# Performance work log

Measured on AMD Instinct MI355X. Metric: run time of the kernel, lower is better.

Reference implementation:

```python
import jax, jax.numpy as jnp
import numpy as np

N_NODES = 50000
N_EDGES = 800000
D_IN = 128
D_HID = 128   # initlial_net_sizes[-1]
D_GC = 128    # gc_out
D_OUT = 256   # feats_out


def setup_inputs() -> dict:
    key = jax.random.key(0)
    ks = jax.random.split(key, 8)
    feats = jax.random.normal(ks[0], (N_NODES, D_IN), dtype=jnp.float32)
    edges = jax.random.randint(ks[1], (2, N_EDGES), 0, N_NODES, dtype=jnp.int64)
    batch = jnp.sort(jax.random.randint(ks[2], (N_NODES,), 0, 64, dtype=jnp.int64))
    s = 0.05
    W1 = jax.random.normal(ks[3], (D_IN, D_HID), dtype=jnp.float32) * s
    b1 = jnp.zeros((D_HID,), dtype=jnp.float32)
    Wg = jax.random.normal(ks[4], (D_HID, D_GC), dtype=jnp.float32) * s
    bg = jnp.zeros((D_GC,), dtype=jnp.float32)
    W2 = jax.random.normal(ks[5], (D_HID + D_GC, D_OUT), dtype=jnp.float32) * s
    b2 = jnp.zeros((D_OUT,), dtype=jnp.float32)
    return {"feats": feats, "edges": edges, "batch": batch,
            "W1": W1, "b1": b1, "Wg": Wg, "bg": bg, "W2": W2, "b2": b2}


def _gcn_conv(x, edges, Wg, bg):
    # PyG GCNConv: linear -> add self-loops -> sym degree norm -> scatter-add -> bias
    n = x.shape[0]
    x = x @ Wg                                   # [N, D_GC]
    loop = jnp.arange(n, dtype=edges.dtype)
    src = jnp.concatenate([edges[0], loop])      # message source (x_j)
    dst = jnp.concatenate([edges[1], loop])      # aggregation target
    deg = jax.ops.segment_sum(jnp.ones_like(dst, dtype=x.dtype), dst, num_segments=n)
    dinv = jnp.where(deg > 0, jax.lax.rsqrt(deg), 0.0)
    norm = dinv[src] * dinv[dst]                 # [E+N]
    msg = x[src] * norm[:, None]                 # [E+N, D_GC]
    out = jax.ops.segment_sum(msg, dst, num_segments=n)
    return out + bg


def reference(feats, edges, batch, W1, b1, Wg, bg, W2, b2):
    nfeats = feats @ W1 + b1                     # fcnn (single Linear, no activation)
    gc_feats = _gcn_conv(nfeats, edges, Wg, bg)  # GCNConv
    combined = jnp.concatenate([nfeats, gc_feats], axis=1) @ W2 + b2
    return (combined, edges, batch)
```

## Files before the change

### kernel.cpp

```cpp
#include <hip/hip_runtime.h>
#include <hip/hip_bf16.h>
#include <stdint.h>


#define NND 50000
#define NE  800000

typedef unsigned int u32;
typedef unsigned short u16;
typedef unsigned long long u64;
typedef short bf16x8 __attribute__((ext_vector_type(8)));
typedef float f32x4  __attribute__((ext_vector_type(4)));

#define OFF_CSR  12800000
#define OFF_RNK  13200000
#define OFF_ROW  13600000
#define OFF_DEG  13700004
#define OFF_DINV 13750004
#define OFF_WPK2 13800004
#define OFF_WPK1 13832772
#define OFF_WPKG 13840964
#define OFF_BSUM 13849156

__device__ __forceinline__ float bf_lo(u32 u) { return __uint_as_float(u << 16); }
__device__ __forceinline__ float bf_hi(u32 u) { return __uint_as_float(u & 0xFFFF0000u); }
__device__ __forceinline__ unsigned short f2b(float f) {
    __hip_bfloat16 h = __float2bfloat16(f);
    return *(unsigned short*)&h;
}
__device__ __forceinline__ u32 pk2(float lo, float hi) {
    return ((u32)f2b(hi) << 16) | (u32)f2b(lo);
}

__device__ __forceinline__ int probe_isbf_par(const u32* p, int stride, int lane) {
    u32 v = p[lane * stride];
    u32 e = (v >> 7) & 0xFFu;
    u64 m = __ballot(e >= 90u && e <= 150u);
    return (__popcll(m) >= 40) ? 1 : 0;
}
__device__ __forceinline__ int probe_intfmt_par(const u32* p, int base, int stride, int lane) {
    int i = lane & 31;
    bool lo = lane < 32;
    u32 a = p[base + i * stride];
    u32 b = p[base + i * stride + 1];
    u32 e1 = (a >> 7) & 0xFFu;
    int small = __popcll(__ballot(lo && a < 50000u))
              + __popcll(__ballot(lo && b < 50000u));
    int oddz  = __popcll(__ballot(lo && b == 0u));
    int bfe   = __popcll(__ballot(lo && e1 >= 110u && e1 <= 145u));
    return (small >= 56) ? ((oddz >= 31) ? 1 : 0) : ((bfe >= 20) ? 3 : 2);
}

__device__ __forceinline__ int iread(const void* p, int fmt, int idx) {
    switch (fmt) {
        case 0:  return ((const int*)p)[idx];
        case 1:  return ((const int*)p)[2 * idx];
        case 2:  return (int)(((const float*)p)[idx] + 0.5f);
        default: return (int)(__bfloat162float(((const __hip_bfloat16*)p)[idx]) + 0.5f);
    }
}
__device__ __forceinline__ float fread_pass(const void* p, int fmt, int idx) {
    switch (fmt) {
        case 0:  return (float)((const int*)p)[idx];
        case 1:  return (float)((const int*)p)[2 * idx];
        case 2:  return ((const float*)p)[idx];
        default: return __bfloat162float(((const __hip_bfloat16*)p)[idx]);
    }
}
__device__ __forceinline__ float rdf(const void* p, int idx, int isbf) {
    return isbf ? __bfloat162float(((const __hip_bfloat16*)p)[idx])
                : ((const float*)p)[idx];
}
__device__ __forceinline__ float rdbias(const void* p, int idx) {
    return __bfloat162float(((const __hip_bfloat16*)p)[idx]);
}

__global__ __launch_bounds__(256) void k_degpack(
    const void* edges, const void* W1, const void* Wg, const void* W2,
    int* __restrict__ deg, u16* __restrict__ rank16,
    u16* __restrict__ Wpk1, u16* __restrict__ Wpkg, u16* __restrict__ Wpk2)
{
    int b = blockIdx.x, tid = threadIdx.x, lane = tid & 63;
    if (b < 3125) {
        int fmt = probe_intfmt_par((const u32*)edges, 0, 24992, lane);
        int e = b * 256 + tid;
        if (e < NE) {
            int s = iread(edges, fmt, e);
            int d = iread(edges, fmt, NE + e);
            if ((u32)s < (u32)NND && (u32)d < (u32)NND) {
                int r = atomicAdd(&deg[d], 1);
                rank16[e] = (u16)r;
            }
        }
    } else if (b < 3189) {
        int wbf = probe_isbf_par((const u32*)W1, 127, lane);
        int idx = (b - 3125) * 256 + tid;
        int j = idx & 7, l = (idx >> 3) & 63, nt = (idx >> 9) & 7, kk = (idx >> 12) & 3;
        int k = kk * 32 + ((l >> 4) & 3) * 8 + j;
        int n = nt * 16 + (l & 15);
        Wpk1[idx] = f2b(rdf(W1, k * 128 + n, wbf));
    } else if (b < 3253) {
        int wbf = probe_isbf_par((const u32*)Wg, 127, lane);
        int idx = (b - 3189) * 256 + tid;
        int j = idx & 7, l = (idx >> 3) & 63, nt = (idx >> 9) & 7, kk = (idx >> 12) & 3;
        int k = kk * 32 + ((l >> 4) & 3) * 8 + j;
        int n = nt * 16 + (l & 15);
        Wpkg[idx] = f2b(rdf(Wg, k * 128 + n, wbf));
    } else {
        int wbf = probe_isbf_par((const u32*)W2, 509, lane);
        int idx = (b - 3253) * 256 + tid;
        int j = idx & 7, l = (idx >> 3) & 63, nt = (idx >> 9) & 15, kk = idx >> 13;
        int k = kk * 32 + ((l >> 4) & 3) * 8 + j;
        int n = nt * 16 + (l & 15);
        Wpk2[idx] = f2b(rdf(W2, k * 256 + n, wbf));
    }
}

__global__ __launch_bounds__(256) void k_scannfxp(
    const int* __restrict__ deg, int* __restrict__ bsum,
    const void* feats, const u32* __restrict__ Wpk1, const u32* __restrict__ Wpkg,
    const void* b1, float* __restrict__ out, int M)
{
    __shared__ alignas(16) u32 smem[2048 + 2176];
    int b = blockIdx.x, tid = threadIdx.x;

    if (b < 196) {
        int* part = (int*)smem;
        int idx = b * 256 + tid;
        part[tid] = (idx < NND) ? deg[idx] : 0;
        __syncthreads();
        for (int off = 128; off >= 1; off >>= 1) {
            if (tid < off) part[tid] += part[tid + off];
            __syncthreads();
        }
        if (tid == 0) bsum[b] = part[0];
        return;
    }

    int nb = b - 196;
    int row0 = nb * 32;
    int lane = tid & 63, w = tid >> 6;
    u32* sApk = smem;
    uint4* sApk4 = (uint4*)smem;
    u16* nfl  = (u16*)(smem + 2048);

    int fbf = probe_isbf_par((const u32*)feats, 997, lane);

    if (fbf) {
        const u32* fw = (const u32*)feats;
        for (int i4 = tid; i4 < 512; i4 += 256) {
            int l = i4 & 63, kk = (i4 >> 6) & 3, mt = (i4 >> 8) & 1;
            int m = mt * 16 + (l & 15);
            int k0b = kk * 32 + ((l >> 4) & 3) * 8;
            int row = row0 + m;
            uint4 v = make_uint4(0u, 0u, 0u, 0u);
            if (row < M) v = *(const uint4*)&fw[(size_t)row * 64 + (k0b >> 1)];
            sApk4[i4] = v;
        }
    } else {
        const float* ff = (const float*)feats;
        for (int i4 = tid; i4 < 512; i4 += 256) {
            int l = i4 & 63, kk = (i4 >> 6) & 3, mt = (i4 >> 8) & 1;
            int m = mt * 16 + (l & 15);
            int k0b = kk * 32 + ((l >> 4) & 3) * 8;
            int row = row0 + m;
            uint4 v = make_uint4(0u, 0u, 0u, 0u);
            if (row < M) {
                float4 fa = *(const float4*)&ff[(size_t)row * 128 + k0b];
                float4 fb = *(const float4*)&ff[(size_t)row * 128 + k0b + 4];
                v = make_uint4(pk2(fa.x, fa.y), pk2(fa.z, fa.w),
                               pk2(fb.x, fb.y), pk2(fb.z, fb.w));
            }
            sApk4[i4] = v;
        }
    }
    __syncthreads();

    f32x4 acc[2][2];
#pragma unroll
    for (int mt = 0; mt < 2; ++mt)
#pragma unroll
        for (int t = 0; t < 2; ++t) acc[mt][t] = (f32x4){0.f, 0.f, 0.f, 0.f};

    for (int kk = 0; kk < 4; ++kk) {
        union { uint4 u; bf16x8 h; } ca0, ca1;
        ca0.u = *(const uint4*)&sApk[(kk * 64 + lane) * 4];
        ca1.u = *(const uint4*)&sApk[((4 + kk) * 64 + lane) * 4];
#pragma unroll
        for (int t = 0; t < 2; ++t) {
            int nt = w * 2 + t;
            union { uint4 u; bf16x8 h; } cb;
            cb.u = *(const uint4*)&Wpk1[((kk * 8 + nt) * 64 + lane) * 4];
            acc[0][t] = __builtin_amdgcn_mfma_f32_16x16x32_bf16(ca0.h, cb.h, acc[0][t], 0, 0, 0);
            acc[1][t] = __builtin_amdgcn_mfma_f32_16x16x32_bf16(ca1.h, cb.h, acc[1][t], 0, 0, 0);
        }
    }

    unsigned short* o16 = (unsigned short*)out;
    int q = lane >> 4, cn = lane & 15;
#pragma unroll
    for (int mt = 0; mt < 2; ++mt)
#pragma unroll
        for (int t = 0; t < 2; ++t) {
            int col = (w * 2 + t) * 16 + cn;
            float bb = rdbias(b1, col);
#pragma unroll
            for (int r = 0; r < 4; ++r) {
                int rowl = mt * 16 + q * 4 + r;
                int row = row0 + rowl;
                unsigned short v = f2b(acc[mt][t][r] + bb);
                nfl[rowl * 136 + col] = v;
                if (row < M) o16[(size_t)row * 512 + col] = v;
            }
        }
    __syncthreads();

    f32x4 acc2[2][2];
#pragma unroll
    for (int mt = 0; mt < 2; ++mt)
#pragma unroll
        for (int t = 0; t < 2; ++t) acc2[mt][t] = (f32x4){0.f, 0.f, 0.f, 0.f};

    for (int kk = 0; kk < 4; ++kk) {
        int kcol = kk * 32 + ((lane >> 4) & 3) * 8;
        union { uint4 u; bf16x8 h; } ca0, ca1;
        ca0.u = *(const uint4*)&nfl[(lane & 15) * 136 + kcol];
        ca1.u = *(const uint4*)&nfl[(16 + (lane & 15)) * 136 + kcol];
#pragma unroll
        for (int t = 0; t < 2; ++t) {
            int nt = w * 2 + t;
            union { uint4 u; bf16x8 h; } cb;
            cb.u = *(const uint4*)&Wpkg[((kk * 8 + nt) * 64 + lane) * 4];
            acc2[0][t] = __builtin_amdgcn_mfma_f32_16x16x32_bf16(ca0.h, cb.h, acc2[0][t], 0, 0, 0);
            acc2[1][t] = __builtin_amdgcn_mfma_f32_16x16x32_bf16(ca1.h, cb.h, acc2[1][t], 0, 0, 0);
        }
    }

#pragma unroll
    for (int mt = 0; mt < 2; ++mt)
#pragma unroll
        for (int t = 0; t < 2; ++t) {
            int col = (w * 2 + t) * 16 + cn;
#pragma unroll
            for (int r = 0; r < 4; ++r) {
                int row = row0 + mt * 16 + q * 4 + r;
                if (row < M)
                    o16[(size_t)row * 512 + 256 + col] = f2b(acc2[mt][t][r]);
            }
        }
}

__global__ __launch_bounds__(256) void k_scan23(
    const int* __restrict__ deg, const int* __restrict__ bsum,
    int* __restrict__ row_start, float* __restrict__ dinv)
{
    __shared__ int part[256];
    __shared__ int sboff;
    int t = threadIdx.x, b = blockIdx.x;

    int v = (t < 196) ? bsum[t] : 0;
    part[t] = v;
    __syncthreads();
    for (int off = 1; off < 256; off <<= 1) {
        int x = (t >= off) ? part[t - off] : 0;
        __syncthreads();
        part[t] += x;
        __syncthreads();
    }
    if (t == b) sboff = part[t] - v;
    if (b == 0 && t == 255) row_start[NND] = part[255];
    __syncthreads();
    int boffb = sboff;
    __syncthreads();

    int idx = b * 256 + t;
    int dv = (idx < NND) ? deg[idx] : 0;
    part[t] = dv;
    __syncthreads();
    for (int off = 1; off < 256; off <<= 1) {
        int x = (t >= off) ? part[t - off] : 0;
        __syncthreads();
        part[t] += x;
        __syncthreads();
    }
    if (idx < NND) {
        int rs = boffb + part[t] - dv;
        row_start[idx] = rs;
        dinv[idx] = rsqrtf((float)(dv + 1));
    }
}

__global__ __launch_bounds__(256) void k_place(const void* edges,
                                               const int* __restrict__ row_start,
                                               const u16* __restrict__ rank16,
                                               u16* __restrict__ csr16)
{
    int fmt = probe_intfmt_par((const u32*)edges, 0, 24992, threadIdx.x & 63);
    int e = blockIdx.x * 256 + threadIdx.x;
    if (e < NE) {
        int s = iread(edges, fmt, e);
        int d = iread(edges, fmt, NE + e);
        if ((u32)s < (u32)NND && (u32)d < (u32)NND) {
            int pos = row_start[d] + (int)rank16[e];
            csr16[pos] = (u16)s;
        }
    }
}

__global__ __launch_bounds__(256) void k_gather(
    const u16* __restrict__ csr16, const int* __restrict__ row_start,
    const float* __restrict__ dinv, const void* bg, u32* __restrict__ uw)
{
    int gt = blockIdx.x * 256 + threadIdx.x;
    int node = gt >> 6, l = gt & 63;
    if (node >= NND) return;
    int beg = row_start[node], end = row_start[node + 1];

    u32 us = uw[(size_t)node * 256 + 128 + l];
    float di = dinv[node];
    float bg0 = rdbias(bg, 2 * l);
    float bg1 = rdbias(bg, 2 * l + 1);

    float a0 = 0.f, a1 = 0.f;
    float c0 = 0.f, c1 = 0.f;
    int e0 = end - 1;
    for (int i = beg; i < end; i += 8) {
        int j1 = i + 1, j2 = i + 2, j3 = i + 3;
        int j4 = i + 4, j5 = i + 5, j6 = i + 6, j7 = i + 7;
        int s0 = csr16[i];
        int s1 = csr16[j1 < e0 ? j1 : e0];
        int s2 = csr16[j2 < e0 ? j2 : e0];
        int s3 = csr16[j3 < e0 ? j3 : e0];
        int s4 = csr16[j4 < e0 ? j4 : e0];
        int s5 = csr16[j5 < e0 ? j5 : e0];
        int s6 = csr16[j6 < e0 ? j6 : e0];
        int s7 = csr16[j7 < e0 ? j7 : e0];
        u32 u0 = uw[(size_t)s0 * 256 + 128 + l];
        u32 u1 = uw[(size_t)s1 * 256 + 128 + l];
        u32 u2 = uw[(size_t)s2 * 256 + 128 + l];
        u32 u3 = uw[(size_t)s3 * 256 + 128 + l];
        u32 u4 = uw[(size_t)s4 * 256 + 128 + l];
        u32 u5 = uw[(size_t)s5 * 256 + 128 + l];
        u32 u6 = uw[(size_t)s6 * 256 + 128 + l];
        u32 u7 = uw[(size_t)s7 * 256 + 128 + l];
        float w0 = dinv[s0];
        float w1 = (j1 <= e0) ? dinv[s1] : 0.f;
        float w2 = (j2 <= e0) ? dinv[s2] : 0.f;
        float w3 = (j3 <= e0) ? dinv[s3] : 0.f;
        float w4 = (j4 <= e0) ? dinv[s4] : 0.f;
        float w5 = (j5 <= e0) ? dinv[s5] : 0.f;
        float w6 = (j6 <= e0) ? dinv[s6] : 0.f;
        float w7 = (j7 <= e0) ? dinv[s7] : 0.f;
        a0 = fmaf(w0, bf_lo(u0), a0); a1 = fmaf(w0, bf_hi(u0), a1);
        c0 = fmaf(w1, bf_lo(u1), c0); c1 = fmaf(w1, bf_hi(u1), c1);
        a0 = fmaf(w2, bf_lo(u2), a0); a1 = fmaf(w2, bf_hi(u2), a1);
        c0 = fmaf(w3, bf_lo(u3), c0); c1 = fmaf(w3, bf_hi(u3), c1);
        a0 = fmaf(w4, bf_lo(u4), a0); a1 = fmaf(w4, bf_hi(u4), a1);
        c0 = fmaf(w5, bf_lo(u5), c0); c1 = fmaf(w5, bf_hi(u5), c1);
        a0 = fmaf(w6, bf_lo(u6), a0); a1 = fmaf(w6, bf_hi(u6), a1);
        c0 = fmaf(w7, bf_lo(u7), c0); c1 = fmaf(w7, bf_hi(u7), c1);
    }
    a0 += c0; a1 += c1;
    float g0 = di * (a0 + di * bf_lo(us)) + bg0;
    float g1 = di * (a1 + di * bf_hi(us)) + bg1;
    uw[(size_t)node * 256 + 192 + l] = ((u32)f2b(g1) << 16) | (u32)f2b(g0);
}

__global__ __launch_bounds__(256) void k_final(
    const u32* __restrict__ Wpk, const void* b2, float* __restrict__ out, int M)
{
    __shared__ alignas(16) u32 sApk[4096];
    uint4* sApk4 = (uint4*)sApk;
    int tid = threadIdx.x;
    int row0 = blockIdx.x * 32;
    const u32* uw = (const u32*)out;

    for (int i4 = tid; i4 < 1024; i4 += 256) {
        int l = i4 & 63, kk = (i4 >> 6) & 7, mt = (i4 >> 9) & 1;
        int m = mt * 16 + (l & 15);
        int k0b = kk * 32 + ((l >> 4) & 3) * 8;
        int row = row0 + m;
        uint4 v = make_uint4(0u, 0u, 0u, 0u);
        if (row < M) {
            size_t base = (kk < 4)
                ? (size_t)row * 256 + (k0b >> 1)
                : (size_t)row * 256 + 192 + ((k0b - 128) >> 1);
            v = *(const uint4*)&uw[base];
        }
        sApk4[i4] = v;
    }
    __syncthreads();

    int w = tid >> 6, lane = tid & 63;
    f32x4 acc[2][4];
#pragma unroll
    for (int mt = 0; mt < 2; ++mt)
#pragma unroll
        for (int t = 0; t < 4; ++t) acc[mt][t] = (f32x4){0.f, 0.f, 0.f, 0.f};

    for (int kk = 0; kk < 8; ++kk) {
        union { uint4 u; bf16x8 h; } ca0, ca1;
        ca0.u = *(const uint4*)&sApk[(kk * 64 + lane) * 4];
        ca1.u = *(const uint4*)&sApk[((8 + kk) * 64 + lane) * 4];
#pragma unroll
        for (int t = 0; t < 4; ++t) {
            int nt = w * 4 + t;
            union { uint4 u; bf16x8 h; } cb;
            cb.u = *(const uint4*)&Wpk[((size_t)(kk * 16 + nt) * 64 + lane) * 4];
            acc[0][t] = __builtin_amdgcn_mfma_f32_16x16x32_bf16(ca0.h, cb.h, acc[0][t], 0, 0, 0);
            acc[1][t] = __builtin_amdgcn_mfma_f32_16x16x32_bf16(ca1.h, cb.h, acc[1][t], 0, 0, 0);
        }
    }

    int q = lane >> 4, cn = lane & 15;
#pragma unroll
    for (int mt = 0; mt < 2; ++mt)
#pragma unroll
        for (int t = 0; t < 4; ++t) {
            int col = w * 64 + t * 16 + cn;
            float bb = rdbias(b2, col);
#pragma unroll
            for (int r = 0; r < 4; ++r) {
                int row = row0 + mt * 16 + q * 4 + r;
                if (row < M) {
                    float v = acc[mt][t][r] + bb;
                    if (!(fabsf(v) < 900.f)) v = (v == v) ? copysignf(900.f, v) : 0.f;
                    out[(size_t)row * 256 + col] = v;
                }
            }
        }
}

__global__ __launch_bounds__(256) void k_tail(
    const void* edges, const void* batch, float* __restrict__ out)
{
    int lane = threadIdx.x & 63;
    int f0 = probe_intfmt_par((const u32*)edges, 0, 24992, lane);
    int f1 = probe_intfmt_par((const u32*)batch, 20000, 156, lane);
    int T = blockIdx.x * 256 + threadIdx.x;
    if (T < NE) {
        size_t o = (size_t)NND * 256 + 2 * (size_t)T;
        if (f0 == 1) {
            int4 v = ((const int4*)edges)[T];
            *(float2*)&out[o] = make_float2((float)v.x, (float)v.z);
        } else {
            out[o]     = fread_pass(edges, f0, 2 * T);
            out[o + 1] = fread_pass(edges, f0, 2 * T + 1);
        }
    } else if (T < NE + NND / 2) {
        int U = T - NE;
        size_t o = (size_t)NND * 256 + 2 * (size_t)NE + 2 * (size_t)U;
        if (f1 == 1) {
            int4 v = ((const int4*)batch)[U];
            *(float2*)&out[o] = make_float2((float)v.x, (float)v.z);
        } else {
            out[o]     = fread_pass(batch, f1, 2 * U);
            out[o + 1] = fread_pass(batch, f1, 2 * U + 1);
        }
    }
}

extern "C" void kernel_launch(void* const* d_in, const int* in_sizes, int n_in,
                              void* d_out, int out_size, void* d_ws, size_t ws_size,
                              hipStream_t stream)
{
    int i_feats = -1, i_edges = -1, i_batch = -1, i_W1 = -1, i_Wg = -1,
        i_W2 = -1, i_b1 = -1, i_bg = -1, i_b2 = -1;
    for (int i = 0; i < n_in; ++i) {
        int s = in_sizes[i];
        if      (s == 6400000) i_feats = i;
        else if (s == 1600000) i_edges = i;
        else if (s == 50000)   i_batch = i;
        else if (s == 65536)   i_W2 = i;
        else if (s == 256)     i_b2 = i;
        else if (s == 16384)   { if (i_W1 < 0) i_W1 = i; else i_Wg = i; }
        else if (s == 128)     { if (i_b1 < 0) i_b1 = i; else i_bg = i; }
    }
    if (i_feats < 0 || i_edges < 0 || i_batch < 0 || i_W1 < 0 || i_Wg < 0 ||
        i_W2 < 0 || i_b1 < 0 || i_bg < 0 || i_b2 < 0) {
        i_feats = 0; i_edges = 1; i_batch = 2; i_W1 = 3; i_b1 = 4;
        i_Wg = 5; i_bg = 6; i_W2 = 7; i_b2 = 8;
    }
    const void* feats = d_in[i_feats];
    const void* edges = d_in[i_edges];
    const void* batch = d_in[i_batch];
    const void* W1 = d_in[i_W1];
    const void* b1 = d_in[i_b1];
    const void* Wg = d_in[i_Wg];
    const void* bg = d_in[i_bg];
    const void* W2 = d_in[i_W2];
    const void* b2 = d_in[i_b2];

    float* out = (float*)d_out;
    u16*   csr16     = (u16*)  (out + OFF_CSR);
    u16*   rank16    = (u16*)  (out + OFF_RNK);
    int*   row_start = (int*)  (out + OFF_ROW);
    int*   deg       = (int*)  (out + OFF_DEG);
    float* dinv      = (float*)(out + OFF_DINV);
    u16*   Wpk2 = (u16*)(out + OFF_WPK2);
    u16*   Wpk1 = (u16*)(out + OFF_WPK1);
    u16*   Wpkg = (u16*)(out + OFF_WPKG);
    int*   bsum = (int*)(out + OFF_BSUM);

    hipMemsetAsync(deg, 0, 200000, stream);
    k_degpack <<<3509,  256, 0, stream>>>(edges, W1, Wg, W2, deg, rank16,
                                          Wpk1, Wpkg, Wpk2);
    k_scannfxp<<<1759,  256, 0, stream>>>(deg, bsum, feats, (const u32*)Wpk1,
                                          (const u32*)Wpkg, b1, out, NND);
    k_scan23  <<<196,   256, 0, stream>>>(deg, bsum, row_start, dinv);
    k_place   <<<3125,  256, 0, stream>>>(edges, row_start, rank16, csr16);
    k_gather  <<<12500, 256, 0, stream>>>(csr16, row_start, dinv, bg, (u32*)out);
    k_final   <<<1563,  256, 0, stream>>>((const u32*)Wpk2, b2, out, NND);
    k_tail    <<<3224,  256, 0, stream>>>(edges, batch, out);
}
```

Measured before the change: 221.7 us.

## Restructure prologue kernels: fold memset into weight pack, merge degree count with node GEMM

Weight packing and zeroing the degree array now run together in a small kernel ahead of everything else, replacing the separate memset. Degree counting now shares a launch with the feature/GCN-linear GEMM, because that GEMM only needs the packed weights and not the degrees. The block-sum pass is removed: each scan block recomputes its prefix offset by summing all earlier degree chunks directly. This removes one launch and one memset, at the cost of scan blocks doing redundant reads whose amount grows with block index.

```diff
diff --git a/kernel.cpp b/kernel.cpp
--- a/kernel.cpp
+++ b/kernel.cpp
@@ -20,7 +20,6 @@
 #define OFF_WPK2 13800004
 #define OFF_WPK1 13832772
 #define OFF_WPKG 13840964
-#define OFF_BSUM 13849156
 
 __device__ __forceinline__ float bf_lo(u32 u) { return __uint_as_float(u << 16); }
 __device__ __forceinline__ float bf_hi(u32 u) { return __uint_as_float(u & 0xFFFF0000u); }
@@ -75,12 +74,48 @@
     return __bfloat162float(((const __hip_bfloat16*)p)[idx]);
 }
 
-__global__ __launch_bounds__(256) void k_degpack(
-    const void* edges, const void* W1, const void* Wg, const void* W2,
+__global__ __launch_bounds__(256) void k_pack(
+    const void* W1, const void* Wg, const void* W2,
+    u16* __restrict__ Wpk1, u16* __restrict__ Wpkg, u16* __restrict__ Wpk2,
+    int* __restrict__ deg)
+{
+    int b = blockIdx.x, tid = threadIdx.x, lane = tid & 63;
+    if (b < 64) {
+        int wbf = probe_isbf_par((const u32*)W1, 127, lane);
+        int idx = b * 256 + tid;
+        int j = idx & 7, l = (idx >> 3) & 63, nt = (idx >> 9) & 7, kk = (idx >> 12) & 3;
+        int k = kk * 32 + ((l >> 4) & 3) * 8 + j;
+        int n = nt * 16 + (l & 15);
+        Wpk1[idx] = f2b(rdf(W1, k * 128 + n, wbf));
+    } else if (b < 128) {
+        int wbf = probe_isbf_par((const u32*)Wg, 127, lane);
+        int idx = (b - 64) * 256 + tid;
+        int j = idx & 7, l = (idx >> 3) & 63, nt = (idx >> 9) & 7, kk = (idx >> 12) & 3;
+        int k = kk * 32 + ((l >> 4) & 3) * 8 + j;
+        int n = nt * 16 + (l & 15);
+        Wpkg[idx] = f2b(rdf(Wg, k * 128 + n, wbf));
+    } else if (b < 384) {
+        int wbf = probe_isbf_par((const u32*)W2, 509, lane);
+        int idx = (b - 128) * 256 + tid;
+        int j = idx & 7, l = (idx >> 3) & 63, nt = (idx >> 9) & 15, kk = idx >> 13;
+        int k = kk * 32 + ((l >> 4) & 3) * 8 + j;
+        int n = nt * 16 + (l & 15);
+        Wpk2[idx] = f2b(rdf(W2, k * 256 + n, wbf));
+    } else {
+        int idx = (b - 384) * 256 + tid;
+        if (idx < 12500) ((int4*)deg)[idx] = make_int4(0, 0, 0, 0);
+    }
+}
+
+__global__ __launch_bounds__(256) void k_degnfxp(
+    const void* edges, const void* feats,
+    const u32* __restrict__ Wpk1, const u32* __restrict__ Wpkg, const void* b1,
     int* __restrict__ deg, u16* __restrict__ rank16,
-    u16* __restrict__ Wpk1, u16* __restrict__ Wpkg, u16* __restrict__ Wpk2)
-{
+    float* __restrict__ out, int M)
+{
+    __shared__ alignas(16) u32 smem[2048 + 2176];
     int b = blockIdx.x, tid = threadIdx.x, lane = tid & 63;
+
     if (b < 3125) {
         int fmt = probe_intfmt_par((const u32*)edges, 0, 24992, lane);
         int e = b * 256 + tid;
@@ -92,54 +127,12 @@
                 rank16[e] = (u16)r;
             }
         }
-    } else if (b < 3189) {
-        int wbf = probe_isbf_par((const u32*)W1, 127, lane);
-        int idx = (b - 3125) * 256 + tid;
-        int j = idx & 7, l = (idx >> 3) & 63, nt = (idx >> 9) & 7, kk = (idx >> 12) & 3;
-        int k = kk * 32 + ((l >> 4) & 3) * 8 + j;
-        int n = nt * 16 + (l & 15);
-        Wpk1[idx] = f2b(rdf(W1, k * 128 + n, wbf));
-    } else if (b < 3253) {
-        int wbf = probe_isbf_par((const u32*)Wg, 127, lane);
-        int idx = (b - 3189) * 256 + tid;
-        int j = idx & 7, l = (idx >> 3) & 63, nt = (idx >> 9) & 7, kk = (idx >> 12) & 3;
-        int k = kk * 32 + ((l >> 4) & 3) * 8 + j;
-        int n = nt * 16 + (l & 15);
-        Wpkg[idx] = f2b(rdf(Wg, k * 128 + n, wbf));
-    } else {
-        int wbf = probe_isbf_par((const u32*)W2, 509, lane);
-        int idx = (b - 3253) * 256 + tid;
-        int j = idx & 7, l = (idx >> 3) & 63, nt = (idx >> 9) & 15, kk = idx >> 13;
-        int k = kk * 32 + ((l >> 4) & 3) * 8 + j;
-        int n = nt * 16 + (l & 15);
-        Wpk2[idx] = f2b(rdf(W2, k * 256 + n, wbf));
-    }
-}
-
-__global__ __launch_bounds__(256) void k_scannfxp(
-    const int* __restrict__ deg, int* __restrict__ bsum,
-    const void* feats, const u32* __restrict__ Wpk1, const u32* __restrict__ Wpkg,
-    const void* b1, float* __restrict__ out, int M)
-{
-    __shared__ alignas(16) u32 smem[2048 + 2176];
-    int b = blockIdx.x, tid = threadIdx.x;
-
-    if (b < 196) {
-        int* part = (int*)smem;
-        int idx = b * 256 + tid;
-        part[tid] = (idx < NND) ? deg[idx] : 0;
-        __syncthreads();
-        for (int off = 128; off >= 1; off >>= 1) {
-            if (tid < off) part[tid] += part[tid + off];
-            __syncthreads();
-        }
-        if (tid == 0) bsum[b] = part[0];
         return;
     }
 
-    int nb = b - 196;
+    int nb = b - 3125;
     int row0 = nb * 32;
-    int lane = tid & 63, w = tid >> 6;
+    int w = tid >> 6;
     u32* sApk = smem;
     uint4* sApk4 = (uint4*)smem;
     u16* nfl  = (u16*)(smem + 2048);
@@ -250,16 +243,30 @@
         }
 }
 
-__global__ __launch_bounds__(256) void k_scan23(
-    const int* __restrict__ deg, const int* __restrict__ bsum,
+__global__ __launch_bounds__(256) void k_scan(
+    const int* __restrict__ deg,
     int* __restrict__ row_start, float* __restrict__ dinv)
 {
     __shared__ int part[256];
-    __shared__ int sboff;
+    __shared__ int stot;
     int t = threadIdx.x, b = blockIdx.x;
 
-    int v = (t < 196) ? bsum[t] : 0;
-    part[t] = v;
+    int acc = 0;
+    for (int c = 0; c < b; ++c) acc += deg[c * 256 + t];
+    part[t] = acc;
+    __syncthreads();
+    for (int off = 128; off >= 1; off >>= 1) {
+        if (t < off) part[t] += part[t + off];
+        __syncthreads();
+    }
+    if (t == 0) stot = part[0];
+    __syncthreads();
+    int S_b = stot;
+    __syncthreads();
+
+    int idx = b * 256 + t;
+    int dv = (idx < NND) ? deg[idx] : 0;
+    part[t] = dv;
     __syncthreads();
     for (int off = 1; off < 256; off <<= 1) {
         int x = (t >= off) ? part[t - off] : 0;
@@ -267,27 +274,12 @@
         part[t] += x;
         __syncthreads();
     }
-    if (t == b) sboff = part[t] - v;
-    if (b == 0 && t == 255) row_start[NND] = part[255];
-    __syncthreads();
-    int boffb = sboff;
-    __syncthreads();
-
-    int idx = b * 256 + t;
-    int dv = (idx < NND) ? deg[idx] : 0;
-    part[t] = dv;
-    __syncthreads();
-    for (int off = 1; off < 256; off <<= 1) {
-        int x = (t >= off) ? part[t - off] : 0;
-        __syncthreads();
-        part[t] += x;
-        __syncthreads();
-    }
     if (idx < NND) {
-        int rs = boffb + part[t] - dv;
+        int rs = S_b + part[t] - dv;
         row_start[idx] = rs;
         dinv[idx] = rsqrtf((float)(dv + 1));
     }
+    if (b == 195 && t == 255) row_start[NND] = S_b + part[255];
 }
 
 __global__ __launch_bounds__(256) void k_place(const void* edges,
@@ -500,14 +492,12 @@
     u16*   Wpk2 = (u16*)(out + OFF_WPK2);
     u16*   Wpk1 = (u16*)(out + OFF_WPK1);
     u16*   Wpkg = (u16*)(out + OFF_WPKG);
-    int*   bsum = (int*)(out + OFF_BSUM);
-
-    hipMemsetAsync(deg, 0, 200000, stream);
-    k_degpack <<<3509,  256, 0, stream>>>(edges, W1, Wg, W2, deg, rank16,
-                                          Wpk1, Wpkg, Wpk2);
-    k_scannfxp<<<1759,  256, 0, stream>>>(deg, bsum, feats, (const u32*)Wpk1,
-                                          (const u32*)Wpkg, b1, out, NND);
-    k_scan23  <<<196,   256, 0, stream>>>(deg, bsum, row_start, dinv);
+
+    k_pack    <<<433,   256, 0, stream>>>(W1, Wg, W2, Wpk1, Wpkg, Wpk2, deg);
+    k_degnfxp <<<4688,  256, 0, stream>>>(edges, feats, (const u32*)Wpk1,
+                                          (const u32*)Wpkg, b1, deg, rank16,
+                                          out, NND);
+    k_scan    <<<196,   256, 0, stream>>>(deg, row_start, dinv);
     k_place   <<<3125,  256, 0, stream>>>(edges, row_start, rank16, csr16);
     k_gather  <<<12500, 256, 0, stream>>>(csr16, row_start, dinv, bg, (u32*)out);
     k_final   <<<1563,  256, 0, stream>>>((const u32*)Wpk2, b2, out, NND);
```

Result: slower. 248.7 us (+12.2%).
